# Optimization experiments

Hardware: AMD Instinct MI355X
Metric: run time of the kernel (lower is better)

## Reference

```python
import jax, jax.numpy as jnp
import numpy as np

N_NODES = 50000
N_EDGES = 800000
VOCAB = 100000
EMB = 64
HID = 64
N_CLASSES = 10
N_GRAPHS = 512


def setup_inputs() -> dict:
    key = jax.random.key(0)
    ks = jax.random.split(key, 12)
    node_ids = jax.random.randint(ks[0], (N_NODES,), 0, VOCAB)
    edge_index = jax.random.randint(ks[1], (2, N_EDGES), 0, N_NODES)
    batch = jnp.sort(jax.random.randint(ks[2], (N_NODES,), 0, N_GRAPHS))
    emb = jax.random.normal(ks[3], (VOCAB, EMB), jnp.float32)
    s_e = 1.0 / np.sqrt(EMB)
    s_h = 1.0 / np.sqrt(HID)
    Wl0 = jax.random.normal(ks[4], (EMB, HID), jnp.float32) * s_e
    bl0 = jnp.zeros((HID,), jnp.float32)
    Wr0 = jax.random.normal(ks[5], (EMB, HID), jnp.float32) * s_e
    Wl1 = jax.random.normal(ks[6], (HID, HID), jnp.float32) * s_h
    bl1 = jnp.zeros((HID,), jnp.float32)
    Wr1 = jax.random.normal(ks[7], (HID, HID), jnp.float32) * s_h
    Wout = jax.random.normal(ks[8], (HID, N_CLASSES), jnp.float32) * s_h
    bout = jnp.zeros((N_CLASSES,), jnp.float32)
    return {"node_ids": node_ids, "edge_index": edge_index, "batch": batch,
            "emb": emb, "Wl0": Wl0, "bl0": bl0, "Wr0": Wr0,
            "Wl1": Wl1, "bl1": bl1, "Wr1": Wr1, "Wout": Wout, "bout": bout}


def _sage_conv(x, src, dst, Wl, bl, Wr):
    # PyG SAGEConv (aggr='mean'): out_i = lin_l(mean_{j in N(i)} x_j) + lin_r(x_i)
    msg = x[src]                                      # [E, d] gather
    s = jax.ops.segment_sum(msg, dst, num_segments=N_NODES)
    cnt = jax.ops.segment_sum(jnp.ones((msg.shape[0], 1), x.dtype), dst,
                              num_segments=N_NODES)
    mean = jnp.where(cnt > 0, s / jnp.maximum(cnt, 1), 0)
    return mean @ Wl + bl + x @ Wr


def reference(node_ids, edge_index, batch, emb, Wl0, bl0, Wr0, Wl1, bl1, Wr1, Wout, bout):
    x = emb[node_ids]                                  # [N, EMB]
    src, dst = edge_index[0], edge_index[1]
    x = jax.nn.relu(_sage_conv(x, src, dst, Wl0, bl0, Wr0))
    x = jax.nn.relu(_sage_conv(x, src, dst, Wl1, bl1, Wr1))
    # global_mean_pool over graph ids
    s = jax.ops.segment_sum(x, batch, num_segments=N_GRAPHS)
    cnt = jax.ops.segment_sum(jnp.ones((x.shape[0], 1), x.dtype), batch,
                              num_segments=N_GRAPHS)
    pooled = jnp.where(cnt > 0, s / jnp.maximum(cnt, 1), 0)   # [G, HID]
    return pooled @ Wout + bout                        # [G, N_CLASSES]
```

## Files before the change

kernel.cpp:

```cpp
#include <hip/hip_runtime.h>
#include <hip/hip_bf16.h>

#define N_NODES 50000
#define N_EDGES 800000
#define EMB 64
#define HID 64
#define N_CLASSES 10
#define N_GRAPHS 512

#define BKT_SHIFT 6
#define BKT_NODES 64
#define NB_BKT ((N_NODES + BKT_NODES - 1) / BKT_NODES)
#define BKT_CAP 1408
#define EB_CHUNK 2048
#define EB_BLOCKS ((N_EDGES + EB_CHUNK - 1) / EB_CHUNK)
#define XFORM_BLOCKS ((N_NODES + 63) / 64)
#define XPAD 68
#define POOL_SPAN 66

#define ACC8(vv, A)                                                            \
    do {                                                                       \
        A[0] += __uint_as_float((vv).x << 16);                                 \
        A[1] += __uint_as_float((vv).x & 0xFFFF0000u);                         \
        A[2] += __uint_as_float((vv).y << 16);                                 \
        A[3] += __uint_as_float((vv).y & 0xFFFF0000u);                         \
        A[4] += __uint_as_float((vv).z << 16);                                 \
        A[5] += __uint_as_float((vv).z & 0xFFFF0000u);                         \
        A[6] += __uint_as_float((vv).w << 16);                                 \
        A[7] += __uint_as_float((vv).w & 0xFFFF0000u);                         \
    } while (0)

__device__ __forceinline__ void build_local_csr(
    int bucket, const int* __restrict__ cnt, const int* __restrict__ ebuf,
    unsigned short* lcsr, int* nhist, int* sval, int* sexcl, int* ncur) {
    int tid = threadIdx.x;
    int bs = bucket * BKT_CAP;
    int ne = min(cnt[bucket], BKT_CAP);
    if (tid < BKT_NODES) { nhist[tid] = 0; ncur[tid] = 0; }
    __syncthreads();
    for (int i = tid; i < ne; i += 256)
        atomicAdd(&nhist[ebuf[bs + i] >> 16], 1);
    __syncthreads();
    if (tid < BKT_NODES) sval[tid] = nhist[tid];
    __syncthreads();
    for (int off = 1; off < BKT_NODES; off <<= 1) {
        int t = 0;
        if (tid < BKT_NODES && tid >= off) t = nhist[tid - off];
        __syncthreads();
        if (tid < BKT_NODES) nhist[tid] += t;
        __syncthreads();
    }
    if (tid < BKT_NODES) sexcl[tid] = nhist[tid] - sval[tid];
    __syncthreads();
    for (int i = tid; i < ne; i += 256) {
        int p = ebuf[bs + i];
        int l = p >> 16;
        int r = atomicAdd(&ncur[l], 1);
        lcsr[sexcl[l] + r] = (unsigned short)(p & 0xFFFF);
    }
    __syncthreads();
}

__device__ __forceinline__ void agg_node8(
    int s0, int deg, int sl,
    const unsigned short* lcsr,
    const __hip_bfloat16* __restrict__ Pb,
    float out[8]) {
    float a[4][8];
#pragma unroll
    for (int i = 0; i < 4; i++)
#pragma unroll
        for (int j = 0; j < 8; j++) a[i][j] = 0.f;
    int s1 = s0 + deg;
    for (int base = s0; base < s1; base += 8) {
        int c = min(8, s1 - base);
        if (c == 8) {
            int n0 = lcsr[base + 0];
            int n1 = lcsr[base + 1];
            int n2 = lcsr[base + 2];
            int n3 = lcsr[base + 3];
            int n4 = lcsr[base + 4];
            int n5 = lcsr[base + 5];
            int n6 = lcsr[base + 6];
            int n7 = lcsr[base + 7];
            uint4 v0 = ((const uint4*)(Pb + (size_t)n0 * 64))[sl];
            uint4 v1 = ((const uint4*)(Pb + (size_t)n1 * 64))[sl];
            uint4 v2 = ((const uint4*)(Pb + (size_t)n2 * 64))[sl];
            uint4 v3 = ((const uint4*)(Pb + (size_t)n3 * 64))[sl];
            uint4 v4 = ((const uint4*)(Pb + (size_t)n4 * 64))[sl];
            uint4 v5 = ((const uint4*)(Pb + (size_t)n5 * 64))[sl];
            uint4 v6 = ((const uint4*)(Pb + (size_t)n6 * 64))[sl];
            uint4 v7 = ((const uint4*)(Pb + (size_t)n7 * 64))[sl];
            ACC8(v0, a[0]); ACC8(v1, a[1]); ACC8(v2, a[2]); ACC8(v3, a[3]);
            ACC8(v4, a[0]); ACC8(v5, a[1]); ACC8(v6, a[2]); ACC8(v7, a[3]);
        } else {
            for (int j = 0; j < c; j++) {
                int n = lcsr[base + j];
                uint4 v = ((const uint4*)(Pb + (size_t)n * 64))[sl];
                ACC8(v, a[j & 3]);
            }
        }
    }
    float inv = (deg > 0) ? 1.0f / (float)deg : 0.0f;
#pragma unroll
    for (int j = 0; j < 8; j++)
        out[j] = (a[0][j] + a[1][j] + a[2][j] + a[3][j]) * inv;
}

__global__ __launch_bounds__(256) void k_combo(
    const int* __restrict__ esrc, const int* __restrict__ edst,
    int* __restrict__ cnt, int* __restrict__ ebuf,
    const int* __restrict__ ids, const float* __restrict__ emb,
    const float* __restrict__ Wl, const float* __restrict__ bl,
    const float* __restrict__ Wr,
    __hip_bfloat16* __restrict__ Pb, float* __restrict__ Qout) {
    __shared__ float sW[64 * 64];
    __shared__ float sX[64 * XPAD];
    int t = threadIdx.x;
    if (blockIdx.x < EB_BLOCKS) {
        int* h = (int*)sW;
        int* bbase = h + NB_BKT;
        int* cur = (int*)sX;
        for (int i = t; i < NB_BKT; i += 256) { h[i] = 0; cur[i] = 0; }
        __syncthreads();
        int base = blockIdx.x * EB_CHUNK;
        int end = min(base + EB_CHUNK, N_EDGES);
        for (int i = base + t; i < end; i += 256)
            atomicAdd(&h[edst[i] >> BKT_SHIFT], 1);
        __syncthreads();
        for (int i = t; i < NB_BKT; i += 256)
            if (h[i]) bbase[i] = i * BKT_CAP + atomicAdd(&cnt[i], h[i]);
        __syncthreads();
        for (int i = base + t; i < end; i += 256) {
            int d = edst[i], s = esrc[i];
            int b = d >> BKT_SHIFT;
            int r = atomicAdd(&cur[b], 1);
            int slot = bbase[b] + r;
            if (slot < (b + 1) * BKT_CAP)
                ebuf[slot] = ((d & (BKT_NODES - 1)) << 16) | s;
        }
        return;
    }
    int tile = (blockIdx.x - EB_BLOCKS) * 64;
    for (int i = t; i < 64 * 16; i += 256)
        ((float4*)sW)[i] = ((const float4*)Wl)[i];
    for (int i = t; i < 64 * 16; i += 256) {
        int r = i >> 4, c = i & 15;
        int node = tile + r;
        float4 v = make_float4(0.f, 0.f, 0.f, 0.f);
        if (node < N_NODES)
            v = ((const float4*)(emb + (size_t)ids[node] * 64))[c];
        *(float4*)&sX[r * XPAD + c * 4] = v;
    }
    __syncthreads();
    int dg = t & 15, ng = t >> 4;
    float acc[4][4];
#pragma unroll
    for (int i = 0; i < 4; i++)
#pragma unroll
        for (int j = 0; j < 4; j++) acc[i][j] = 0.f;
#pragma unroll 4
    for (int k = 0; k < 64; k++) {
        float4 w = *(const float4*)&sW[k * 64 + dg * 4];
#pragma unroll
        for (int i = 0; i < 4; i++) {
            float xv = sX[(ng + i * 16) * XPAD + k];
            acc[i][0] = fmaf(xv, w.x, acc[i][0]);
            acc[i][1] = fmaf(xv, w.y, acc[i][1]);
            acc[i][2] = fmaf(xv, w.z, acc[i][2]);
            acc[i][3] = fmaf(xv, w.w, acc[i][3]);
        }
    }
#pragma unroll
    for (int i = 0; i < 4; i++) {
        int node = tile + ng + i * 16;
        if (node < N_NODES) {
            union { ushort4 u; __hip_bfloat16 h[4]; } pk;
            pk.h[0] = __float2bfloat16(acc[i][0]);
            pk.h[1] = __float2bfloat16(acc[i][1]);
            pk.h[2] = __float2bfloat16(acc[i][2]);
            pk.h[3] = __float2bfloat16(acc[i][3]);
            *(ushort4*)&Pb[(size_t)node * 64 + dg * 4] = pk.u;
        }
    }
    __syncthreads();
    for (int i = t; i < 64 * 16; i += 256)
        ((float4*)sW)[i] = ((const float4*)Wr)[i];
    __syncthreads();
#pragma unroll
    for (int i = 0; i < 4; i++)
#pragma unroll
        for (int j = 0; j < 4; j++) acc[i][j] = 0.f;
#pragma unroll 4
    for (int k = 0; k < 64; k++) {
        float4 w = *(const float4*)&sW[k * 64 + dg * 4];
#pragma unroll
        for (int i = 0; i < 4; i++) {
            float xv = sX[(ng + i * 16) * XPAD + k];
            acc[i][0] = fmaf(xv, w.x, acc[i][0]);
            acc[i][1] = fmaf(xv, w.y, acc[i][1]);
            acc[i][2] = fmaf(xv, w.z, acc[i][2]);
            acc[i][3] = fmaf(xv, w.w, acc[i][3]);
        }
    }
    float4 blv = *(const float4*)&bl[dg * 4];
#pragma unroll
    for (int i = 0; i < 4; i++) {
        int node = tile + ng + i * 16;
        if (node < N_NODES)
            *(float4*)&Qout[(size_t)node * 64 + dg * 4] =
                make_float4(acc[i][0] + blv.x, acc[i][1] + blv.y,
                            acc[i][2] + blv.z, acc[i][3] + blv.w);
    }
}

__global__ __launch_bounds__(256) void k_fused1(
    const int* __restrict__ cnt, const int* __restrict__ ebuf,
    const __hip_bfloat16* __restrict__ Pb0, const float* __restrict__ Wl,
    const float* __restrict__ bl, const float* __restrict__ Wr,
    __hip_bfloat16* __restrict__ Pb1, float* __restrict__ H) {
    __shared__ float sW[64 * 64];
    __shared__ float sX[64 * XPAD];
    __shared__ unsigned short lcsr[BKT_CAP];
    __shared__ int nhist[BKT_NODES], sval[BKT_NODES], sexcl[BKT_NODES], ncur[BKT_NODES];
    int t = threadIdx.x;
    int tile = blockIdx.x * 64;
    for (int i = t; i < 64 * 16; i += 256)
        ((float4*)sW)[i] = ((const float4*)Wl)[i];
    build_local_csr(blockIdx.x, cnt, ebuf, lcsr, nhist, sval, sexcl, ncur);
    int grp = t >> 3, sl = t & 7;
    for (int nn = 0; nn < 2; nn++) {
        int ln = grp * 2 + nn;
        int node = tile + ln;
        float m[8];
        agg_node8(sexcl[ln], sval[ln], sl, lcsr, Pb0, m);
        if (node < N_NODES) {
            size_t off = (size_t)node * 64 + sl * 8;
            float4 q0 = *(const float4*)&H[off];
            float4 q1 = *(const float4*)&H[off + 4];
            m[0] = fmaxf(m[0] + q0.x, 0.f);
            m[1] = fmaxf(m[1] + q0.y, 0.f);
            m[2] = fmaxf(m[2] + q0.z, 0.f);
            m[3] = fmaxf(m[3] + q0.w, 0.f);
            m[4] = fmaxf(m[4] + q1.x, 0.f);
            m[5] = fmaxf(m[5] + q1.y, 0.f);
            m[6] = fmaxf(m[6] + q1.z, 0.f);
            m[7] = fmaxf(m[7] + q1.w, 0.f);
        } else {
#pragma unroll
            for (int j = 0; j < 8; j++) m[j] = 0.f;
        }
        *(float4*)&sX[ln * XPAD + sl * 8] = make_float4(m[0], m[1], m[2], m[3]);
        *(float4*)&sX[ln * XPAD + sl * 8 + 4] = make_float4(m[4], m[5], m[6], m[7]);
    }
    __syncthreads();
    int dg = t & 15, ng = t >> 4;
    float acc[4][4];
#pragma unroll
    for (int i = 0; i < 4; i++)
#pragma unroll
        for (int j = 0; j < 4; j++) acc[i][j] = 0.f;
#pragma unroll 4
    for (int k = 0; k < 64; k++) {
        float4 w = *(const float4*)&sW[k * 64 + dg * 4];
#pragma unroll
        for (int i = 0; i < 4; i++) {
            float xv = sX[(ng + i * 16) * XPAD + k];
            acc[i][0] = fmaf(xv, w.x, acc[i][0]);
            acc[i][1] = fmaf(xv, w.y, acc[i][1]);
            acc[i][2] = fmaf(xv, w.z, acc[i][2]);
            acc[i][3] = fmaf(xv, w.w, acc[i][3]);
        }
    }
#pragma unroll
    for (int i = 0; i < 4; i++) {
        int node = tile + ng + i * 16;
        if (node < N_NODES) {
            union { ushort4 u; __hip_bfloat16 h[4]; } pk;
            pk.h[0] = __float2bfloat16(acc[i][0]);
            pk.h[1] = __float2bfloat16(acc[i][1]);
            pk.h[2] = __float2bfloat16(acc[i][2]);
            pk.h[3] = __float2bfloat16(acc[i][3]);
            *(ushort4*)&Pb1[(size_t)node * 64 + dg * 4] = pk.u;
        }
    }
    __syncthreads();
    for (int i = t; i < 64 * 16; i += 256)
        ((float4*)sW)[i] = ((const float4*)Wr)[i];
    __syncthreads();
#pragma unroll
    for (int i = 0; i < 4; i++)
#pragma unroll
        for (int j = 0; j < 4; j++) acc[i][j] = 0.f;
#pragma unroll 4
    for (int k = 0; k < 64; k++) {
        float4 w = *(const float4*)&sW[k * 64 + dg * 4];
#pragma unroll
        for (int i = 0; i < 4; i++) {
            float xv = sX[(ng + i * 16) * XPAD + k];
            acc[i][0] = fmaf(xv, w.x, acc[i][0]);
            acc[i][1] = fmaf(xv, w.y, acc[i][1]);
            acc[i][2] = fmaf(xv, w.z, acc[i][2]);
            acc[i][3] = fmaf(xv, w.w, acc[i][3]);
        }
    }
    float4 blv = *(const float4*)&bl[dg * 4];
#pragma unroll
    for (int i = 0; i < 4; i++) {
        int node = tile + ng + i * 16;
        if (node < N_NODES)
            *(float4*)&H[(size_t)node * 64 + dg * 4] =
                make_float4(acc[i][0] + blv.x, acc[i][1] + blv.y,
                            acc[i][2] + blv.z, acc[i][3] + blv.w);
    }
}

__global__ __launch_bounds__(256) void k_agg2_pool(
    const int* __restrict__ cnt, const int* __restrict__ ebuf,
    const __hip_bfloat16* __restrict__ Pb, const float* __restrict__ H,
    const int* __restrict__ batch, float* __restrict__ psum) {
    __shared__ float acc[POOL_SPAN * 64];
    __shared__ unsigned short lcsr[BKT_CAP];
    __shared__ int nhist[BKT_NODES], sval[BKT_NODES], sexcl[BKT_NODES], ncur[BKT_NODES];
    int t = threadIdx.x;
    int nb = blockIdx.x * 64;
    for (int i = t; i < POOL_SPAN * 64; i += 256) acc[i] = 0.f;
    build_local_csr(blockIdx.x, cnt, ebuf, lcsr, nhist, sval, sexcl, ncur);
    int gmin = batch[nb];
    int grp = t >> 3, sl = t & 7;
    for (int nn = 0; nn < 2; nn++) {
        int ln = grp * 2 + nn;
        int node = nb + ln;
        float m[8];
        agg_node8(sexcl[ln], sval[ln], sl, lcsr, Pb, m);
        if (node < N_NODES) {
            size_t off = (size_t)node * 64 + sl * 8;
            float4 q0 = *(const float4*)&H[off];
            float4 q1 = *(const float4*)&H[off + 4];
            m[0] = fmaxf(m[0] + q0.x, 0.f);
            m[1] = fmaxf(m[1] + q0.y, 0.f);
            m[2] = fmaxf(m[2] + q0.z, 0.f);
            m[3] = fmaxf(m[3] + q0.w, 0.f);
            m[4] = fmaxf(m[4] + q1.x, 0.f);
            m[5] = fmaxf(m[5] + q1.y, 0.f);
            m[6] = fmaxf(m[6] + q1.z, 0.f);
            m[7] = fmaxf(m[7] + q1.w, 0.f);
            int g = batch[node];
            int lg = g - gmin;
            if (lg < POOL_SPAN) {
#pragma unroll
                for (int j = 0; j < 8; j++)
                    atomicAdd(&acc[lg * 64 + sl * 8 + j], m[j]);
            } else {
#pragma unroll
                for (int j = 0; j < 8; j++)
                    atomicAdd(&psum[(size_t)g * 64 + sl * 8 + j], m[j]);
            }
        }
    }
    __syncthreads();
    int nlast = min(nb + 63, N_NODES - 1);
    int gspan = min(batch[nlast] - gmin + 1, POOL_SPAN);
    for (int i = t; i < gspan * 64; i += 256) {
        float v = acc[i];
        if (v != 0.f)
            atomicAdd(&psum[(size_t)(gmin + (i >> 6)) * 64 + (i & 63)], v);
    }
}

__device__ __forceinline__ int lower_bound_batch(const int* __restrict__ batch, int val) {
    int lo = 0, hi = N_NODES;
    while (lo < hi) {
        int mid = (lo + hi) >> 1;
        if (batch[mid] < val) lo = mid + 1; else hi = mid;
    }
    return lo;
}

__global__ __launch_bounds__(256) void k_out(
    const int* __restrict__ batch, const float* __restrict__ psum,
    const float* __restrict__ Wout, const float* __restrict__ bout,
    float* __restrict__ out) {
    int w = threadIdx.x >> 6, lane = threadIdx.x & 63;
    int g = blockIdx.x * 4 + w;
    if (g >= N_GRAPHS) return;
    int s0 = lower_bound_batch(batch, g);
    int s1 = lower_bound_batch(batch, g + 1);
    int cntg = s1 - s0;
    float inv = (cntg > 0) ? 1.0f / (float)cntg : 0.0f;
    float pooled = psum[(size_t)g * 64 + lane] * inv;
#pragma unroll
    for (int c = 0; c < N_CLASSES; c++) {
        float v = pooled * Wout[lane * N_CLASSES + c];
#pragma unroll
        for (int off = 32; off > 0; off >>= 1) v += __shfl_down(v, off, 64);
        if (lane == 0) out[(size_t)g * N_CLASSES + c] = v + bout[c];
    }
}


extern "C" void kernel_launch(void* const* d_in, const int* in_sizes, int n_in,
                              void* d_out, int out_size, void* d_ws, size_t ws_size,
                              hipStream_t stream) {
    const int*   node_ids = (const int*)d_in[0];
    const int*   edge_idx = (const int*)d_in[1];
    const int*   batch    = (const int*)d_in[2];
    const float* emb      = (const float*)d_in[3];
    const float* Wl0      = (const float*)d_in[4];
    const float* bl0      = (const float*)d_in[5];
    const float* Wr0      = (const float*)d_in[6];
    const float* Wl1      = (const float*)d_in[7];
    const float* bl1      = (const float*)d_in[8];
    const float* Wr1      = (const float*)d_in[9];
    const float* Wout     = (const float*)d_in[10];
    const float* bout     = (const float*)d_in[11];
    float* out = (float*)d_out;

    const int* esrc = edge_idx;
    const int* edst = edge_idx + N_EDGES;

    __hip_bfloat16* Pb0 = (__hip_bfloat16*)d_ws;
    __hip_bfloat16* Pb1 = Pb0 + (size_t)N_NODES * 64;
    float* H = (float*)(Pb1 + (size_t)N_NODES * 64);
    int* ebuf = (int*)(H + (size_t)N_NODES * 64);
    int* cnt = ebuf + (size_t)NB_BKT * BKT_CAP;
    float* psum = (float*)(cnt + NB_BKT);

    const int BLK = 256;

    hipMemsetAsync(cnt, 0, (NB_BKT + N_GRAPHS * 64) * sizeof(int), stream);

    k_combo<<<EB_BLOCKS + XFORM_BLOCKS, BLK, 0, stream>>>(
        esrc, edst, cnt, ebuf, node_ids, emb, Wl0, bl0, Wr0, Pb0, H);

    k_fused1<<<XFORM_BLOCKS, BLK, 0, stream>>>(cnt, ebuf, Pb0, Wl1, bl1, Wr1, Pb1, H);

    k_agg2_pool<<<NB_BKT, BLK, 0, stream>>>(cnt, ebuf, Pb1, H, batch, psum);

    k_out<<<(N_GRAPHS + 3) / 4, BLK, 0, stream>>>(batch, psum, Wout, bout, out);
}
```

Before: 216.4 us.

## Interleave two-node gathers, pad bucket counters, and replace pool atomics with segmented scan

Several changes ship together. Each thread group now aggregates its two nodes in an interleaved loop so sixteen independent gathers are in flight at once. Bucket counters are padded to 16-int stride to reduce atomic contention on the same cache lines. The CSR prefix sum is replaced with a wavefront shuffle scan, and the edge-bucketing chunk size is doubled. Pooling now writes rows to shared memory and does a per-column segmented sum with fewer global atomics, replacing the many shared-memory atomics, and occupancy hints are added to the launch bounds. The cost is more registers per thread and more workspace for the padded counters.

```diff
diff --git a/kernel.cpp b/kernel.cpp
--- a/kernel.cpp
+++ b/kernel.cpp
@@ -12,11 +12,11 @@
 #define BKT_NODES 64
 #define NB_BKT ((N_NODES + BKT_NODES - 1) / BKT_NODES)
 #define BKT_CAP 1408
-#define EB_CHUNK 2048
+#define CNT_STRIDE 16
+#define EB_CHUNK 4096
 #define EB_BLOCKS ((N_EDGES + EB_CHUNK - 1) / EB_CHUNK)
 #define XFORM_BLOCKS ((N_NODES + 63) / 64)
 #define XPAD 68
-#define POOL_SPAN 66
 
 #define ACC8(vv, A)                                                            \
     do {                                                                       \
@@ -35,22 +35,23 @@
     unsigned short* lcsr, int* nhist, int* sval, int* sexcl, int* ncur) {
     int tid = threadIdx.x;
     int bs = bucket * BKT_CAP;
-    int ne = min(cnt[bucket], BKT_CAP);
+    int ne = min(cnt[bucket * CNT_STRIDE], BKT_CAP);
     if (tid < BKT_NODES) { nhist[tid] = 0; ncur[tid] = 0; }
     __syncthreads();
     for (int i = tid; i < ne; i += 256)
         atomicAdd(&nhist[ebuf[bs + i] >> 16], 1);
     __syncthreads();
-    if (tid < BKT_NODES) sval[tid] = nhist[tid];
-    __syncthreads();
-    for (int off = 1; off < BKT_NODES; off <<= 1) {
-        int t = 0;
-        if (tid < BKT_NODES && tid >= off) t = nhist[tid - off];
-        __syncthreads();
-        if (tid < BKT_NODES) nhist[tid] += t;
-        __syncthreads();
-    }
-    if (tid < BKT_NODES) sexcl[tid] = nhist[tid] - sval[tid];
+    if (tid < 64) {
+        int v = nhist[tid];
+        int s = v;
+#pragma unroll
+        for (int off = 1; off < 64; off <<= 1) {
+            int u = __shfl_up(s, off, 64);
+            if (tid >= off) s += u;
+        }
+        sval[tid] = v;
+        sexcl[tid] = s - v;
+    }
     __syncthreads();
     for (int i = tid; i < ne; i += 256) {
         int p = ebuf[bs + i];
@@ -61,50 +62,85 @@
     __syncthreads();
 }
 
-__device__ __forceinline__ void agg_node8(
-    int s0, int deg, int sl,
-    const unsigned short* lcsr,
-    const __hip_bfloat16* __restrict__ Pb,
-    float out[8]) {
-    float a[4][8];
-#pragma unroll
-    for (int i = 0; i < 4; i++)
-#pragma unroll
-        for (int j = 0; j < 8; j++) a[i][j] = 0.f;
-    int s1 = s0 + deg;
-    for (int base = s0; base < s1; base += 8) {
-        int c = min(8, s1 - base);
-        if (c == 8) {
-            int n0 = lcsr[base + 0];
-            int n1 = lcsr[base + 1];
-            int n2 = lcsr[base + 2];
-            int n3 = lcsr[base + 3];
-            int n4 = lcsr[base + 4];
-            int n5 = lcsr[base + 5];
-            int n6 = lcsr[base + 6];
-            int n7 = lcsr[base + 7];
-            uint4 v0 = ((const uint4*)(Pb + (size_t)n0 * 64))[sl];
-            uint4 v1 = ((const uint4*)(Pb + (size_t)n1 * 64))[sl];
-            uint4 v2 = ((const uint4*)(Pb + (size_t)n2 * 64))[sl];
-            uint4 v3 = ((const uint4*)(Pb + (size_t)n3 * 64))[sl];
-            uint4 v4 = ((const uint4*)(Pb + (size_t)n4 * 64))[sl];
-            uint4 v5 = ((const uint4*)(Pb + (size_t)n5 * 64))[sl];
-            uint4 v6 = ((const uint4*)(Pb + (size_t)n6 * 64))[sl];
-            uint4 v7 = ((const uint4*)(Pb + (size_t)n7 * 64))[sl];
-            ACC8(v0, a[0]); ACC8(v1, a[1]); ACC8(v2, a[2]); ACC8(v3, a[3]);
-            ACC8(v4, a[0]); ACC8(v5, a[1]); ACC8(v6, a[2]); ACC8(v7, a[3]);
-        } else {
-            for (int j = 0; j < c; j++) {
-                int n = lcsr[base + j];
-                uint4 v = ((const uint4*)(Pb + (size_t)n * 64))[sl];
-                ACC8(v, a[j & 3]);
-            }
-        }
-    }
-    float inv = (deg > 0) ? 1.0f / (float)deg : 0.0f;
-#pragma unroll
-    for (int j = 0; j < 8; j++)
-        out[j] = (a[0][j] + a[1][j] + a[2][j] + a[3][j]) * inv;
+__device__ __forceinline__ void agg2(
+    int sA, int dA, int sB, int dB, int sl,
+    const unsigned short* lcsr, const __hip_bfloat16* __restrict__ Pb,
+    float oA[8], float oB[8]) {
+    float a0[8], a1[8], b0[8], b1[8];
+#pragma unroll
+    for (int j = 0; j < 8; j++) { a0[j] = 0.f; a1[j] = 0.f; b0[j] = 0.f; b1[j] = 0.f; }
+    int eA = sA + dA, eB = sB + dB;
+    int pA = sA, pB = sB;
+    while ((pA + 8 <= eA) && (pB + 8 <= eB)) {
+        uint4 vA[8], vB[8];
+#pragma unroll
+        for (int j = 0; j < 8; j++)
+            vA[j] = ((const uint4*)(Pb + (size_t)lcsr[pA + j] * 64))[sl];
+#pragma unroll
+        for (int j = 0; j < 8; j++)
+            vB[j] = ((const uint4*)(Pb + (size_t)lcsr[pB + j] * 64))[sl];
+#pragma unroll
+        for (int j = 0; j < 8; j++) ACC8(vA[j], ((j & 1) ? a1 : a0));
+#pragma unroll
+        for (int j = 0; j < 8; j++) ACC8(vB[j], ((j & 1) ? b1 : b0));
+        pA += 8; pB += 8;
+    }
+    while (pA + 8 <= eA) {
+        uint4 v[8];
+#pragma unroll
+        for (int j = 0; j < 8; j++)
+            v[j] = ((const uint4*)(Pb + (size_t)lcsr[pA + j] * 64))[sl];
+#pragma unroll
+        for (int j = 0; j < 8; j++) ACC8(v[j], ((j & 1) ? a1 : a0));
+        pA += 8;
+    }
+    while (pB + 8 <= eB) {
+        uint4 v[8];
+#pragma unroll
+        for (int j = 0; j < 8; j++)
+            v[j] = ((const uint4*)(Pb + (size_t)lcsr[pB + j] * 64))[sl];
+#pragma unroll
+        for (int j = 0; j < 8; j++) ACC8(v[j], ((j & 1) ? b1 : b0));
+        pB += 8;
+    }
+    for (; pA < eA; ++pA) {
+        uint4 v = ((const uint4*)(Pb + (size_t)lcsr[pA] * 64))[sl];
+        ACC8(v, a0);
+    }
+    for (; pB < eB; ++pB) {
+        uint4 v = ((const uint4*)(Pb + (size_t)lcsr[pB] * 64))[sl];
+        ACC8(v, b0);
+    }
+    float invA = (dA > 0) ? 1.0f / (float)dA : 0.0f;
+    float invB = (dB > 0) ? 1.0f / (float)dB : 0.0f;
+#pragma unroll
+    for (int j = 0; j < 8; j++) {
+        oA[j] = (a0[j] + a1[j]) * invA;
+        oB[j] = (b0[j] + b1[j]) * invB;
+    }
+}
+
+__device__ __forceinline__ void finish_row(int node, int sl,
+                                           const float* __restrict__ H,
+                                           float m[8], float* dst) {
+    if (node < N_NODES) {
+        size_t off = (size_t)node * 64 + sl * 8;
+        float4 q0 = *(const float4*)&H[off];
+        float4 q1 = *(const float4*)&H[off + 4];
+        m[0] = fmaxf(m[0] + q0.x, 0.f);
+        m[1] = fmaxf(m[1] + q0.y, 0.f);
+        m[2] = fmaxf(m[2] + q0.z, 0.f);
+        m[3] = fmaxf(m[3] + q0.w, 0.f);
+        m[4] = fmaxf(m[4] + q1.x, 0.f);
+        m[5] = fmaxf(m[5] + q1.y, 0.f);
+        m[6] = fmaxf(m[6] + q1.z, 0.f);
+        m[7] = fmaxf(m[7] + q1.w, 0.f);
+    } else {
+#pragma unroll
+        for (int j = 0; j < 8; j++) m[j] = 0.f;
+    }
+    *(float4*)&dst[sl * 8] = make_float4(m[0], m[1], m[2], m[3]);
+    *(float4*)&dst[sl * 8 + 4] = make_float4(m[4], m[5], m[6], m[7]);
 }
 
 __global__ __launch_bounds__(256) void k_combo(
@@ -129,7 +165,7 @@
             atomicAdd(&h[edst[i] >> BKT_SHIFT], 1);
         __syncthreads();
         for (int i = t; i < NB_BKT; i += 256)
-            if (h[i]) bbase[i] = i * BKT_CAP + atomicAdd(&cnt[i], h[i]);
+            if (h[i]) bbase[i] = i * BKT_CAP + atomicAdd(&cnt[i * CNT_STRIDE], h[i]);
         __syncthreads();
         for (int i = base + t; i < end; i += 256) {
             int d = edst[i], s = esrc[i];
@@ -214,7 +250,7 @@
     }
 }
 
-__global__ __launch_bounds__(256) void k_fused1(
+__global__ __launch_bounds__(256, 4) void k_fused1(
     const int* __restrict__ cnt, const int* __restrict__ ebuf,
     const __hip_bfloat16* __restrict__ Pb0, const float* __restrict__ Wl,
     const float* __restrict__ bl, const float* __restrict__ Wr,
@@ -229,30 +265,11 @@
         ((float4*)sW)[i] = ((const float4*)Wl)[i];
     build_local_csr(blockIdx.x, cnt, ebuf, lcsr, nhist, sval, sexcl, ncur);
     int grp = t >> 3, sl = t & 7;
-    for (int nn = 0; nn < 2; nn++) {
-        int ln = grp * 2 + nn;
-        int node = tile + ln;
-        float m[8];
-        agg_node8(sexcl[ln], sval[ln], sl, lcsr, Pb0, m);
-        if (node < N_NODES) {
-            size_t off = (size_t)node * 64 + sl * 8;
-            float4 q0 = *(const float4*)&H[off];
-            float4 q1 = *(const float4*)&H[off + 4];
-            m[0] = fmaxf(m[0] + q0.x, 0.f);
-            m[1] = fmaxf(m[1] + q0.y, 0.f);
-            m[2] = fmaxf(m[2] + q0.z, 0.f);
-            m[3] = fmaxf(m[3] + q0.w, 0.f);
-            m[4] = fmaxf(m[4] + q1.x, 0.f);
-            m[5] = fmaxf(m[5] + q1.y, 0.f);
-            m[6] = fmaxf(m[6] + q1.z, 0.f);
-            m[7] = fmaxf(m[7] + q1.w, 0.f);
-        } else {
-#pragma unroll
-            for (int j = 0; j < 8; j++) m[j] = 0.f;
-        }
-        *(float4*)&sX[ln * XPAD + sl * 8] = make_float4(m[0], m[1], m[2], m[3]);
-        *(float4*)&sX[ln * XPAD + sl * 8 + 4] = make_float4(m[4], m[5], m[6], m[7]);
-    }
+    int ln0 = grp * 2, ln1 = ln0 + 1;
+    float mA[8], mB[8];
+    agg2(sexcl[ln0], sval[ln0], sexcl[ln1], sval[ln1], sl, lcsr, Pb0, mA, mB);
+    finish_row(tile + ln0, sl, H, mA, &sX[ln0 * XPAD]);
+    finish_row(tile + ln1, sl, H, mB, &sX[ln1 * XPAD]);
     __syncthreads();
     int dg = t & 15, ng = t >> 4;
     float acc[4][4];
@@ -315,57 +332,45 @@
     }
 }
 
-__global__ __launch_bounds__(256) void k_agg2_pool(
+__global__ __launch_bounds__(256, 4) void k_agg2_pool(
     const int* __restrict__ cnt, const int* __restrict__ ebuf,
     const __hip_bfloat16* __restrict__ Pb, const float* __restrict__ H,
     const int* __restrict__ batch, float* __restrict__ psum) {
-    __shared__ float acc[POOL_SPAN * 64];
+    __shared__ float sPool[64 * 64];
     __shared__ unsigned short lcsr[BKT_CAP];
     __shared__ int nhist[BKT_NODES], sval[BKT_NODES], sexcl[BKT_NODES], ncur[BKT_NODES];
+    __shared__ int sLg[64];
     int t = threadIdx.x;
     int nb = blockIdx.x * 64;
-    for (int i = t; i < POOL_SPAN * 64; i += 256) acc[i] = 0.f;
+    int gmin = batch[nb];
+    if (t < 64) {
+        int node = nb + t;
+        sLg[t] = batch[node < N_NODES ? node : (N_NODES - 1)] - gmin;
+    }
     build_local_csr(blockIdx.x, cnt, ebuf, lcsr, nhist, sval, sexcl, ncur);
-    int gmin = batch[nb];
     int grp = t >> 3, sl = t & 7;
-    for (int nn = 0; nn < 2; nn++) {
-        int ln = grp * 2 + nn;
-        int node = nb + ln;
-        float m[8];
-        agg_node8(sexcl[ln], sval[ln], sl, lcsr, Pb, m);
-        if (node < N_NODES) {
-            size_t off = (size_t)node * 64 + sl * 8;
-            float4 q0 = *(const float4*)&H[off];
-            float4 q1 = *(const float4*)&H[off + 4];
-            m[0] = fmaxf(m[0] + q0.x, 0.f);
-            m[1] = fmaxf(m[1] + q0.y, 0.f);
-            m[2] = fmaxf(m[2] + q0.z, 0.f);
-            m[3] = fmaxf(m[3] + q0.w, 0.f);
-            m[4] = fmaxf(m[4] + q1.x, 0.f);
-            m[5] = fmaxf(m[5] + q1.y, 0.f);
-            m[6] = fmaxf(m[6] + q1.z, 0.f);
-            m[7] = fmaxf(m[7] + q1.w, 0.f);
-            int g = batch[node];
-            int lg = g - gmin;
-            if (lg < POOL_SPAN) {
-#pragma unroll
-                for (int j = 0; j < 8; j++)
-                    atomicAdd(&acc[lg * 64 + sl * 8 + j], m[j]);
-            } else {
-#pragma unroll
-                for (int j = 0; j < 8; j++)
-                    atomicAdd(&psum[(size_t)g * 64 + sl * 8 + j], m[j]);
-            }
-        }
-    }
-    __syncthreads();
-    int nlast = min(nb + 63, N_NODES - 1);
-    int gspan = min(batch[nlast] - gmin + 1, POOL_SPAN);
-    for (int i = t; i < gspan * 64; i += 256) {
-        float v = acc[i];
-        if (v != 0.f)
-            atomicAdd(&psum[(size_t)(gmin + (i >> 6)) * 64 + (i & 63)], v);
-    }
+    int ln0 = grp * 2, ln1 = ln0 + 1;
+    float mA[8], mB[8];
+    agg2(sexcl[ln0], sval[ln0], sexcl[ln1], sval[ln1], sl, lcsr, Pb, mA, mB);
+    finish_row(nb + ln0, sl, H, mA, &sPool[ln0 * 64]);
+    finish_row(nb + ln1, sl, H, mB, &sPool[ln1 * 64]);
+    __syncthreads();
+    int d = t & 63, q = t >> 6;
+    int n0 = q * 16;
+    float run = 0.f;
+    int cur = sLg[n0];
+    for (int n = n0; n < n0 + 16; n++) {
+        int lg = sLg[n];
+        if (lg != cur) {
+            if (run != 0.f)
+                atomicAdd(&psum[(size_t)(gmin + cur) * 64 + d], run);
+            run = 0.f;
+            cur = lg;
+        }
+        run += sPool[n * 64 + d];
+    }
+    if (run != 0.f)
+        atomicAdd(&psum[(size_t)(gmin + cur) * 64 + d], run);
 }
 
 __device__ __forceinline__ int lower_bound_batch(const int* __restrict__ batch, int val) {
@@ -424,11 +429,11 @@
     float* H = (float*)(Pb1 + (size_t)N_NODES * 64);
     int* ebuf = (int*)(H + (size_t)N_NODES * 64);
     int* cnt = ebuf + (size_t)NB_BKT * BKT_CAP;
-    float* psum = (float*)(cnt + NB_BKT);
+    float* psum = (float*)(cnt + (size_t)NB_BKT * CNT_STRIDE);
 
     const int BLK = 256;
 
-    hipMemsetAsync(cnt, 0, (NB_BKT + N_GRAPHS * 64) * sizeof(int), stream);
+    hipMemsetAsync(cnt, 0, (NB_BKT * CNT_STRIDE + N_GRAPHS * 64) * sizeof(int), stream);
 
     k_combo<<<EB_BLOCKS + XFORM_BLOCKS, BLK, 0, stream>>>(
         esrc, edst, cnt, ebuf, node_ids, emb, Wl0, bl0, Wr0, Pb0, H);
```

Result: faster. 190.1 us (-12.1%).
